# Kernel tuning notes

Measured on AMD Instinct MI355X. Metric: run time of the kernel, lower is better.

Reference implementation:

```python
import jax, jax.numpy as jnp
import numpy as np

B, S, E = 4, 2048, 512
H, D = 8, 64  # n_head, attn_dim


def setup_inputs() -> dict:
    key = jax.random.key(0)
    ks = jax.random.split(key, 12)
    scale = 0.02
    return {
        "input_q": jax.random.normal(ks[0], (B, S, E), dtype=jnp.float32),
        "input_k": jax.random.normal(ks[1], (B, S, E), dtype=jnp.float32),
        "input_v": jax.random.normal(ks[2], (B, S, E), dtype=jnp.float32),
        "mask": jax.random.randint(ks[3], (B, S, S), 0, 2, dtype=jnp.int32),
        "wq": jax.random.normal(ks[4], (E, H * D), dtype=jnp.float32) * scale,
        "bq": jnp.zeros((H * D,), dtype=jnp.float32),
        "wk": jax.random.normal(ks[5], (E, H * D), dtype=jnp.float32) * scale,
        "bk": jnp.zeros((H * D,), dtype=jnp.float32),
        "wv": jax.random.normal(ks[6], (E, H * D), dtype=jnp.float32) * scale,
        "bv": jnp.zeros((H * D,), dtype=jnp.float32),
        "wo": jax.random.normal(ks[7], (H * D, E), dtype=jnp.float32) * scale,
        "bo": jnp.zeros((E,), dtype=jnp.float32),
    }


def reference(input_q, input_k, input_v, mask, wq, bq, wk, bk, wv, bv, wo, bo):
    b, lq, _ = input_q.shape
    lk = input_k.shape[1]
    # projections -> [b, len, H, D] -> [b, H, len, D]
    q = (input_q @ wq + bq).reshape(b, lq, H, D).transpose(0, 2, 1, 3)
    k = (input_k @ wk + bk).reshape(b, lk, H, D).transpose(0, 2, 1, 3)
    v = (input_v @ wv + bv).reshape(b, lk, H, D).transpose(0, 2, 1, 3)
    # raw scores [b, H, lq, lk]
    score = jnp.einsum("bhqd,bhkd->bhqk", q, k)
    # NOTE: original masks with -1e9 BEFORE dividing by sqrt(attn_dim)
    score = jnp.where(mask[:, None, :, :] == 0, jnp.float32(-1e9), score)
    attn = jax.nn.softmax(score / jnp.sqrt(jnp.float32(D)), axis=-1)
    out = jnp.einsum("bhqk,bhkd->bqhd", attn, v).reshape(b, lq, H * D)
    return out @ wo + bo
```

## Files before the change

### kernel.cpp

```cpp
#include <hip/hip_runtime.h>
#include <hip/hip_bf16.h>
#include <hip/hip_fp16.h>
#include <stdint.h>

#define Bc 4
#define Sc 2048
#define Ec 512
#define Hc 8
#define Dc 64
#define HDc 512

typedef __attribute__((ext_vector_type(8))) short bf16x8;
typedef __attribute__((ext_vector_type(2))) _Float16 f16x2;
typedef __attribute__((ext_vector_type(4))) _Float16 f16x4;
typedef __attribute__((ext_vector_type(8))) _Float16 f16x8;
typedef __attribute__((ext_vector_type(4))) float f32x4;
typedef __attribute__((ext_vector_type(16))) float f32x16;
typedef unsigned int u32;

__device__ __forceinline__ unsigned short f2bf(float x) {
    union { float f; unsigned u; } v; v.f = x;
    unsigned r = v.u + 0x7FFFu + ((v.u >> 16) & 1u);
    return (unsigned short)(r >> 16);
}

__device__ __forceinline__ unsigned pkbf2(float a, float b) {
    float2 f; f.x = a; f.y = b;
    __hip_bfloat162 h = __float22bfloat162_rn(f);
    union { __hip_bfloat162 h2; unsigned u; } u; u.h2 = h;
    return u.u;
}

__device__ __forceinline__ unsigned short f2h(float x) {
    return __half_as_ushort(__float2half_rn(x));
}

__device__ __forceinline__ unsigned pkh2(float a, float b) {
    union { __half2 h2; unsigned u; } u;
    u.h2 = __floats2half2_rn(a, b);
    return u.u;
}

__device__ __forceinline__ uint4 pack8(float4 a, float4 b) {
    uint4 v;
    v.x = pkbf2(a.x, a.y); v.y = pkbf2(a.z, a.w);
    v.z = pkbf2(b.x, b.y); v.w = pkbf2(b.z, b.w);
    return v;
}

__device__ __forceinline__ void gload_lds(const void* g, void* l) {
    __builtin_amdgcn_global_load_lds(
        (const __attribute__((address_space(1))) u32*)g,
        (__attribute__((address_space(3))) u32*)l,
        16, 0, 0);
}

__global__ __launch_bounds__(256) void prep(
    const int* __restrict__ mask, unsigned long long* __restrict__ bits,
    const float* __restrict__ W0, const float* __restrict__ W1,
    const float* __restrict__ W2, const float* __restrict__ W3,
    unsigned short* __restrict__ Wt,
    const float* __restrict__ Xq, const float* __restrict__ Xk,
    const float* __restrict__ Xv, unsigned short* __restrict__ Xb)
{
    const int blk = blockIdx.x;
    __shared__ float t[64][65];
    if (blk < 256) {
        const int z = blk >> 6;
        const float* W = z == 0 ? W0 : (z == 1 ? W1 : (z == 2 ? W2 : W3));
        unsigned short* O = Wt + (size_t)z * Ec * HDc;
        const int k0 = ((blk >> 3) & 7) * 64, n0 = (blk & 7) * 64;
#pragma unroll
        for (int i = 0; i < 16; i++) {
            int idx = threadIdx.x + 256 * i;
            int kr = idx >> 6, nc = idx & 63;
            t[nc][kr] = W[(size_t)(k0 + kr) * HDc + n0 + nc];
        }
        __syncthreads();
#pragma unroll
        for (int i = 0; i < 16; i++) {
            int idx = threadIdx.x + 256 * i;
            int nr = idx >> 6, kc = idx & 63;
            O[(size_t)(n0 + nr) * Ec + k0 + kc] = f2bf(t[nr][kc]);
        }
    } else if (blk < 2304) {
        const int lane = threadIdx.x & 63;
        int wave = ((blk - 256) * 256 + (int)threadIdx.x) >> 6;
        const int nwaves = (2048 * 256) >> 6;
        const int nwords = (Bc * Sc * Sc) / 64;
        for (int w = wave; w < nwords; w += nwaves) {
            int m = mask[(size_t)w * 64 + lane];
            unsigned long long b = __ballot(m != 0);
            if (lane == 0) bits[w] = b;
        }
    } else {
        const int zi = blk - 2304;
        const int z = zi >> 11, wi = zi & 2047;
        const float* X = z == 0 ? Xq : (z == 1 ? Xk : Xv);
        const size_t off = ((size_t)wi * 256 + threadIdx.x) * 8;
        const float4* p = (const float4*)(X + off);
        float4 f0 = p[0], f1 = p[1];
        *(uint4*)(Xb + (size_t)z * 4194304 + off) = pack8(f0, f1);
    }
}

__global__ __launch_bounds__(256) void proj_gemm(
    const unsigned short* __restrict__ Xb, const unsigned short* __restrict__ Wt,
    const float* __restrict__ bq, const float* __restrict__ bk, const float* __restrict__ bv,
    unsigned short* __restrict__ Oq, unsigned short* __restrict__ Ok,
    unsigned short* __restrict__ Vt)
{
    const int z = blockIdx.z;
    const unsigned short* Xz = Xb + (size_t)z * 4194304;
    const unsigned short* Bt = Wt + (size_t)z * Ec * HDc;
    const float* bias = z == 0 ? bq : (z == 1 ? bk : bv);

    const int n0 = blockIdx.x * 128;
    const int m0 = blockIdx.y * 128;
    const int tid = threadIdx.x, lane = tid & 63, w = tid >> 6;
    const int c = lane & 15, quad = lane >> 4;
    const int wm = w & 1, wn = w >> 1;

    __shared__ unsigned short As[128 * 64];
    __shared__ unsigned short Bs[128 * 64];

    f32x4 acc[4][4];
#pragma unroll
    for (int i = 0; i < 4; i++)
#pragma unroll
        for (int j = 0; j < 4; j++) acc[i][j] = (f32x4){0.f, 0.f, 0.f, 0.f};

    for (int k0 = 0; k0 < Ec; k0 += 64) {
        __syncthreads();
#pragma unroll
        for (int jj = 0; jj < 4; jj++) {
            int rb = w * 32 + jj * 8;
            int row = rb + (lane >> 3);
            int dg = (lane & 7) ^ (row & 7);
            gload_lds(Bt + (size_t)(n0 + row) * Ec + k0 + dg * 8, &Bs[rb * 64]);
            gload_lds(Xz + (size_t)(m0 + row) * Ec + k0 + dg * 8, &As[rb * 64]);
        }
        __syncthreads();
#pragma unroll
        for (int ks = 0; ks < 2; ks++) {
            int kg = ks * 4 + quad;
            bf16x8 af[4], bfr[4];
#pragma unroll
            for (int mt = 0; mt < 4; mt++) {
                int row = wm * 64 + mt * 16 + c;
                af[mt] = *(const bf16x8*)&As[row * 64 + ((kg ^ (row & 7)) * 8)];
            }
#pragma unroll
            for (int nt = 0; nt < 4; nt++) {
                int row = wn * 64 + nt * 16 + c;
                bfr[nt] = *(const bf16x8*)&Bs[row * 64 + ((kg ^ (row & 7)) * 8)];
            }
            if (z < 2) {
#pragma unroll
                for (int mt = 0; mt < 4; mt++)
#pragma unroll
                    for (int nt = 0; nt < 4; nt++)
                        acc[mt][nt] = __builtin_amdgcn_mfma_f32_16x16x32_bf16(af[mt], bfr[nt], acc[mt][nt], 0, 0, 0);
            } else {
#pragma unroll
                for (int mt = 0; mt < 4; mt++)
#pragma unroll
                    for (int nt = 0; nt < 4; nt++)
                        acc[mt][nt] = __builtin_amdgcn_mfma_f32_16x16x32_bf16(bfr[nt], af[mt], acc[mt][nt], 0, 0, 0);
            }
        }
    }

    if (z < 2) {
        unsigned short* O = z == 0 ? Oq : Ok;
        const float qs = z == 0 ? 0.125f : 1.0f;
#pragma unroll
        for (int mt = 0; mt < 4; mt++)
#pragma unroll
            for (int r = 0; r < 4; r++) {
                int gm = m0 + wm * 64 + mt * 16 + quad * 4 + r;
#pragma unroll
                for (int nt = 0; nt < 4; nt++) {
                    int gn = n0 + wn * 64 + nt * 16 + c;
                    O[(size_t)gm * HDc + gn] = f2bf((acc[mt][nt][r] + bias[gn]) * qs);
                }
            }
    } else {
#pragma unroll
        for (int mt = 0; mt < 4; mt++) {
            int gm = m0 + wm * 64 + mt * 16 + c;
            int bb = gm >> 11, sPos = gm & (Sc - 1);
#pragma unroll
            for (int nt = 0; nt < 4; nt++)
#pragma unroll
                for (int r = 0; r < 4; r++) {
                    int ng = n0 + wn * 64 + nt * 16 + quad * 4 + r;
                    int hh = ng >> 6, d = ng & 63;
                    Vt[((size_t)(bb * Hc + hh) * Dc + d) * Sc + sPos] = f2h(acc[mt][nt][r] + bias[ng]);
                }
        }
    }
}

__global__ __launch_bounds__(256, 4) void attn_kernel(
    const unsigned short* __restrict__ Qb, const unsigned short* __restrict__ Kb,
    const unsigned short* __restrict__ Vt, const unsigned long long* __restrict__ Mb,
    unsigned short* __restrict__ Ob)
{
    const int flat = blockIdx.x + 32 * blockIdx.y + 256 * blockIdx.z;
    const int hb = flat & 7;
    const int qt = (flat >> 3) & 31;
    const int b  = flat >> 8;
    const int q0 = qt * 64;
    const int tid = threadIdx.x, lane = tid & 63, w = tid >> 6;
    const int l31 = lane & 31, hf = lane >> 5;
    const int half = w >> 1;
    const int qgrp = w & 1;

    __shared__ unsigned short SM[16384];
    unsigned short* KsH = SM + half * 4096;
    unsigned short* VsH = SM + 8192 + half * 4096;

    const int qg = q0 + qgrp * 32 + l31;
    const size_t qoff = ((size_t)b * Sc + qg) * HDc + hb * Dc;

    bf16x8 qf[4];
#pragma unroll
    for (int s4 = 0; s4 < 4; s4++)
        qf[s4] = *(const bf16x8*)(Qb + qoff + s4 * 16 + hf * 8);

    const unsigned long long* mr = Mb + ((size_t)b * Sc + qg) * (Sc / 64);
    const size_t kbase = ((size_t)b * Sc) * HDc + hb * Dc;
    const size_t vbase = ((size_t)(b * Hc + hb)) * Dc * Sc;

    f32x16 o[2];
#pragma unroll
    for (int i = 0; i < 16; i++) { o[0][i] = 0.f; o[1][i] = 0.f; }
    float os[4] = {0.f, 0.f, 0.f, 0.f};
    const f16x2 one2 = {(_Float16)1.0f, (_Float16)1.0f};

    auto stage = [&](int t) {
#pragma unroll
        for (int jj = 0; jj < 4; jj++) {
            int rb = qgrp * 32 + jj * 8;
            int row = rb + (lane >> 3);
            int dg = (lane & 7) ^ (row & 7);
            gload_lds(Kb + kbase + (size_t)(t * 64 + row) * HDc + dg * 8, &KsH[rb * 64]);
            gload_lds(Vt + vbase + (size_t)row * Sc + t * 64 + dg * 8, &VsH[rb * 64]);
        }
    };

    for (int i = 0; i < 16; i++) {
        const int t = half * 16 + i;
        unsigned long long mw = mr[t];
        stage(t);
        __syncthreads();

        u32 P16[2][8];
#pragma unroll
        for (int a = 0; a < 2; a++) {
            f32x16 s;
#pragma unroll
            for (int i2 = 0; i2 < 16; i2++) s[i2] = 0.f;
            const int tk = a * 32 + l31;
#pragma unroll
            for (int s4 = 0; s4 < 4; s4++) {
                bf16x8 kf = *(const bf16x8*)&KsH[tk * 64 + (((2 * s4 + hf) ^ (tk & 7)) * 8)];
                s = __builtin_amdgcn_mfma_f32_32x32x16_bf16(kf, qf[s4], s, 0, 0, 0);
            }
            u32 mwa = (a == 0) ? (u32)mw : (u32)(mw >> 32);
            int mq = (int)(mwa >> (4 * hf));
#pragma unroll
            for (int g = 0; g < 4; g++) {
                float p[4];
#pragma unroll
                for (int r = 0; r < 4; r++) {
                    const int pos = 8 * g + r;
                    int keep = __builtin_amdgcn_sbfe(mq, pos, 1);
                    float e = __expf(s[4 * g + r]);
                    p[r] = __int_as_float(__float_as_int(e) & keep);
                }
                u32 u0 = pkh2(p[0], p[1]);
                u32 u1 = pkh2(p[2], p[3]);
                P16[a][2 * g + 0] = u0;
                P16[a][2 * g + 1] = u1;
                union { u32 u; f16x2 h; } d0, d1;
                d0.u = u0; d1.u = u1;
                os[g] = __builtin_amdgcn_fdot2(d0.h, one2, os[g], false);
                os[g] = __builtin_amdgcn_fdot2(d1.h, one2, os[g], false);
            }
        }

        u32 pw[4][4];
#pragma unroll
        for (int s4 = 0; s4 < 4; s4++) {
            const int a = s4 >> 1, base = 4 * (s4 & 1);
#pragma unroll
            for (int pp = 0; pp < 2; pp++) {
                u32 A0 = P16[a][base + pp];
                u32 B1 = P16[a][base + 2 + pp];
                u32 sent = hf ? A0 : B1;
                u32 got = (u32)__shfl_xor((int)sent, 32, 64);
                pw[s4][pp]     = hf ? got : A0;
                pw[s4][2 + pp] = hf ? B1  : got;
            }
        }
#pragma unroll
        for (int s4 = 0; s4 < 4; s4++) {
            union { u32 u[4]; f16x8 v; } pf;
            pf.u[0] = pw[s4][0]; pf.u[1] = pw[s4][1];
            pf.u[2] = pw[s4][2]; pf.u[3] = pw[s4][3];
#pragma unroll
            for (int dt = 0; dt < 2; dt++) {
                const int d = dt * 32 + l31;
                f16x8 vf = *(const f16x8*)&VsH[d * 64 + (((2 * s4 + hf) ^ (d & 7)) * 8)];
                o[dt] = __builtin_amdgcn_mfma_f32_32x32x16_f16(vf, pf.v, o[dt], 0, 0, 0);
            }
        }
        __syncthreads();
    }

    float osum = os[0] + os[1] + os[2] + os[3];
    osum += __shfl_xor(osum, 32, 64);

    float* mbuf = (float*)SM;
    if (half == 1) {
        float* mp = mbuf + (qgrp * 64 + lane) * 34;
#pragma unroll
        for (int dt = 0; dt < 2; dt++)
#pragma unroll
            for (int i = 0; i < 16; i++) mp[dt * 16 + i] = o[dt][i];
        mp[32] = osum;
    }
    __syncthreads();
    if (half == 0) {
        const float* mp = mbuf + (qgrp * 64 + lane) * 34;
#pragma unroll
        for (int dt = 0; dt < 2; dt++)
#pragma unroll
            for (int i = 0; i < 16; i++) o[dt][i] += mp[dt * 16 + i];
        const float inv = 1.0f / (osum + mp[32]);
#pragma unroll
        for (int dt = 0; dt < 2; dt++)
#pragma unroll
            for (int g = 0; g < 4; g++) {
                const int d = dt * 32 + 8 * g + 4 * hf;
                uint2 pk;
                pk.x = pkbf2(o[dt][4 * g + 0] * inv, o[dt][4 * g + 1] * inv);
                pk.y = pkbf2(o[dt][4 * g + 2] * inv, o[dt][4 * g + 3] * inv);
                *(uint2*)(Ob + qoff + d) = pk;
            }
    }
}

__global__ __launch_bounds__(256) void out_gemm(
    const unsigned short* __restrict__ Ab, const unsigned short* __restrict__ Bt,
    const float* __restrict__ bias, float* __restrict__ Out)
{
    const int n0 = blockIdx.x * 128;
    const int m0 = blockIdx.y * 64;
    const int tid = threadIdx.x, lane = tid & 63, w = tid >> 6;
    const int c = lane & 15, quad = lane >> 4;
    const int wm = w & 1, wn = w >> 1;

    __shared__ unsigned short As[64 * 64];
    __shared__ unsigned short Bs[128 * 64];

    f32x4 acc[2][4];
#pragma unroll
    for (int i = 0; i < 2; i++)
#pragma unroll
        for (int j = 0; j < 4; j++) acc[i][j] = (f32x4){0.f, 0.f, 0.f, 0.f};

    for (int k0 = 0; k0 < HDc; k0 += 64) {
        __syncthreads();
#pragma unroll
        for (int jj = 0; jj < 4; jj++) {
            int rb = w * 32 + jj * 8;
            int row = rb + (lane >> 3);
            int dg = (lane & 7) ^ (row & 7);
            gload_lds(Bt + (size_t)(n0 + row) * Ec + k0 + dg * 8, &Bs[rb * 64]);
        }
#pragma unroll
        for (int jj = 0; jj < 2; jj++) {
            int rb = w * 16 + jj * 8;
            int row = rb + (lane >> 3);
            int dg = (lane & 7) ^ (row & 7);
            gload_lds(Ab + (size_t)(m0 + row) * HDc + k0 + dg * 8, &As[rb * 64]);
        }
        __syncthreads();
#pragma unroll
        for (int ks = 0; ks < 2; ks++) {
            int kg = ks * 4 + quad;
            bf16x8 af[2], bfr[4];
#pragma unroll
            for (int mt = 0; mt < 2; mt++) {
                int row = wm * 32 + mt * 16 + c;
                af[mt] = *(const bf16x8*)&As[row * 64 + ((kg ^ (row & 7)) * 8)];
            }
#pragma unroll
            for (int nt = 0; nt < 4; nt++) {
                int row = wn * 64 + nt * 16 + c;
                bfr[nt] = *(const bf16x8*)&Bs[row * 64 + ((kg ^ (row & 7)) * 8)];
            }
#pragma unroll
            for (int mt = 0; mt < 2; mt++)
#pragma unroll
                for (int nt = 0; nt < 4; nt++)
                    acc[mt][nt] = __builtin_amdgcn_mfma_f32_16x16x32_bf16(af[mt], bfr[nt], acc[mt][nt], 0, 0, 0);
        }
    }
#pragma unroll
    for (int mt = 0; mt < 2; mt++)
#pragma unroll
        for (int r = 0; r < 4; r++) {
            int gm = m0 + wm * 32 + mt * 16 + quad * 4 + r;
#pragma unroll
            for (int nt = 0; nt < 4; nt++) {
                int gn = n0 + wn * 64 + nt * 16 + c;
                Out[(size_t)gm * Ec + gn] = acc[mt][nt][r] + bias[gn];
            }
        }
}

extern "C" void kernel_launch(void* const* d_in, const int* in_sizes, int n_in,
                              void* d_out, int out_size, void* d_ws, size_t ws_size,
                              hipStream_t stream)
{
    const float* xq = (const float*)d_in[0];
    const float* xk = (const float*)d_in[1];
    const float* xv = (const float*)d_in[2];
    const int* mask = (const int*)d_in[3];
    const float* wq = (const float*)d_in[4];
    const float* bq = (const float*)d_in[5];
    const float* wk = (const float*)d_in[6];
    const float* bk = (const float*)d_in[7];
    const float* wv = (const float*)d_in[8];
    const float* bv = (const float*)d_in[9];
    const float* wo = (const float*)d_in[10];
    const float* bo = (const float*)d_in[11];
    float* out = (float*)d_out;

    char* ws = (char*)d_ws;
    const size_t MB = 1024 * 1024;
    unsigned short* qb = (unsigned short*)(ws + 0 * MB);
    unsigned short* kb = (unsigned short*)(ws + 8 * MB);
    unsigned short* vt = (unsigned short*)(ws + 16 * MB);
    unsigned short* xb = (unsigned short*)(ws + 24 * MB);
    unsigned short* ab = (unsigned short*)(ws + 24 * MB);
    unsigned long long* mb = (unsigned long long*)(ws + 48 * MB);
    unsigned short* wt = (unsigned short*)(ws + 50 * MB);

    hipLaunchKernelGGL(prep, dim3(8448), dim3(256), 0, stream,
                       mask, mb, wq, wk, wv, wo, wt, xq, xk, xv, xb);

    hipLaunchKernelGGL(proj_gemm, dim3(4, 64, 3), dim3(256), 0, stream,
                       xb, wt, bq, bk, bv, qb, kb, vt);

    hipLaunchKernelGGL(attn_kernel, dim3(32, 8, 4), dim3(256), 0, stream,
                       qb, kb, vt, mb, ab);

    hipLaunchKernelGGL(out_gemm, dim3(4, 128), dim3(256), 0, stream,
                       ab, wt + 3 * (size_t)Ec * HDc, bo, out);
}
```

Baseline: 269.2 us.

## Double-buffer K/V tiles in attention with smaller key tiles and exp2 softmax

```diff
diff --git a/kernel.cpp b/kernel.cpp
--- a/kernel.cpp
+++ b/kernel.cpp
@@ -173,7 +173,7 @@
 
     if (z < 2) {
         unsigned short* O = z == 0 ? Oq : Ok;
-        const float qs = z == 0 ? 0.125f : 1.0f;
+        const float qs = z == 0 ? 0.18033688011112043f : 1.0f;
 #pragma unroll
         for (int mt = 0; mt < 4; mt++)
 #pragma unroll
@@ -218,8 +218,8 @@
     const int qgrp = w & 1;
 
     __shared__ unsigned short SM[16384];
-    unsigned short* KsH = SM + half * 4096;
-    unsigned short* VsH = SM + 8192 + half * 4096;
+    unsigned short* Kb0 = SM + half * 4096;
+    unsigned short* Vb0 = SM + 8192 + half * 4096;
 
     const int qg = q0 + qgrp * 32 + l31;
     const size_t qoff = ((size_t)b * Sc + qg) * HDc + hb * Dc;
@@ -229,9 +229,10 @@
     for (int s4 = 0; s4 < 4; s4++)
         qf[s4] = *(const bf16x8*)(Qb + qoff + s4 * 16 + hf * 8);
 
-    const unsigned long long* mr = Mb + ((size_t)b * Sc + qg) * (Sc / 64);
+    const u32* mr32 = (const u32*)(Mb + ((size_t)b * Sc + qg) * (Sc / 64));
     const size_t kbase = ((size_t)b * Sc) * HDc + hb * Dc;
     const size_t vbase = ((size_t)(b * Hc + hb)) * Dc * Sc;
+    const int tok0 = half * 1024;
 
     f32x16 o[2];
 #pragma unroll
@@ -239,86 +240,102 @@
     float os[4] = {0.f, 0.f, 0.f, 0.f};
     const f16x2 one2 = {(_Float16)1.0f, (_Float16)1.0f};
 
-    auto stage = [&](int t) {
-#pragma unroll
-        for (int jj = 0; jj < 4; jj++) {
-            int rb = qgrp * 32 + jj * 8;
-            int row = rb + (lane >> 3);
-            int dg = (lane & 7) ^ (row & 7);
-            gload_lds(Kb + kbase + (size_t)(t * 64 + row) * HDc + dg * 8, &KsH[rb * 64]);
-            gload_lds(Vt + vbase + (size_t)row * Sc + t * 64 + dg * 8, &VsH[rb * 64]);
+    auto stage = [&](int t, int buf) {
+        unsigned short* Kd = Kb0 + buf * 2048;
+        unsigned short* Vd = Vb0 + buf * 2048;
+#pragma unroll
+        for (int jj = 0; jj < 2; jj++) {
+            int rbk = qgrp * 16 + jj * 8;
+            int rowk = rbk + (lane >> 3);
+            int dgk = (lane & 7) ^ (rowk & 7);
+            gload_lds(Kb + kbase + (size_t)(tok0 + t * 32 + rowk) * HDc + dgk * 8,
+                      &Kd[rbk * 64]);
+            int rbv = qgrp * 32 + jj * 16;
+            int rowd = rbv + (lane >> 2);
+            int dgv = (lane & 3) ^ ((rowd >> 1) & 3);
+            gload_lds(Vt + vbase + (size_t)rowd * Sc + tok0 + t * 32 + dgv * 8,
+                      &Vd[rbv * 32]);
         }
     };
 
-    for (int i = 0; i < 16; i++) {
-        const int t = half * 16 + i;
-        unsigned long long mw = mr[t];
-        stage(t);
-        __syncthreads();
-
-        u32 P16[2][8];
-#pragma unroll
-        for (int a = 0; a < 2; a++) {
-            f32x16 s;
-#pragma unroll
-            for (int i2 = 0; i2 < 16; i2++) s[i2] = 0.f;
-            const int tk = a * 32 + l31;
-#pragma unroll
-            for (int s4 = 0; s4 < 4; s4++) {
-                bf16x8 kf = *(const bf16x8*)&KsH[tk * 64 + (((2 * s4 + hf) ^ (tk & 7)) * 8)];
-                s = __builtin_amdgcn_mfma_f32_32x32x16_bf16(kf, qf[s4], s, 0, 0, 0);
-            }
-            u32 mwa = (a == 0) ? (u32)mw : (u32)(mw >> 32);
-            int mq = (int)(mwa >> (4 * hf));
-#pragma unroll
-            for (int g = 0; g < 4; g++) {
-                float p[4];
-#pragma unroll
-                for (int r = 0; r < 4; r++) {
-                    const int pos = 8 * g + r;
-                    int keep = __builtin_amdgcn_sbfe(mq, pos, 1);
-                    float e = __expf(s[4 * g + r]);
-                    p[r] = __int_as_float(__float_as_int(e) & keep);
-                }
-                u32 u0 = pkh2(p[0], p[1]);
-                u32 u1 = pkh2(p[2], p[3]);
-                P16[a][2 * g + 0] = u0;
-                P16[a][2 * g + 1] = u1;
-                union { u32 u; f16x2 h; } d0, d1;
-                d0.u = u0; d1.u = u1;
-                os[g] = __builtin_amdgcn_fdot2(d0.h, one2, os[g], false);
-                os[g] = __builtin_amdgcn_fdot2(d1.h, one2, os[g], false);
-            }
-        }
-
-        u32 pw[4][4];
+    stage(0, 0);
+    u32 mw_cur = mr32[half * 32];
+    u32 mw_nxt = 0;
+#pragma unroll 2
+    for (int i = 0; i < 32; i++) {
+        const int cur = i & 1;
+        __syncthreads();
+        if (i + 1 < 32) {
+            stage(i + 1, cur ^ 1);
+            mw_nxt = mr32[half * 32 + i + 1];
+        }
+        const unsigned short* Kt = Kb0 + cur * 2048;
+        const unsigned short* Vl = Vb0 + cur * 2048;
+
+        f32x16 s;
+#pragma unroll
+        for (int i2 = 0; i2 < 16; i2++) s[i2] = 0.f;
+        __builtin_amdgcn_s_setprio(1);
 #pragma unroll
         for (int s4 = 0; s4 < 4; s4++) {
-            const int a = s4 >> 1, base = 4 * (s4 & 1);
+            bf16x8 kf = *(const bf16x8*)&Kt[l31 * 64 + (((2 * s4 + hf) ^ (l31 & 7)) * 8)];
+            s = __builtin_amdgcn_mfma_f32_32x32x16_bf16(kf, qf[s4], s, 0, 0, 0);
+        }
+        __builtin_amdgcn_s_setprio(0);
+
+        int mq = (int)(mw_cur >> (4 * hf));
+        u32 P16[8];
+#pragma unroll
+        for (int g = 0; g < 4; g++) {
+            float p[4];
+#pragma unroll
+            for (int r = 0; r < 4; r++) {
+                const int pos = 8 * g + r;
+                int keep = __builtin_amdgcn_sbfe(mq, pos, 1);
+                float e = __builtin_exp2f(s[4 * g + r]);
+                p[r] = __int_as_float(__float_as_int(e) & keep);
+            }
+            u32 u0 = pkh2(p[0], p[1]);
+            u32 u1 = pkh2(p[2], p[3]);
+            P16[2 * g + 0] = u0;
+            P16[2 * g + 1] = u1;
+            union { u32 u; f16x2 h; } d0, d1;
+            d0.u = u0; d1.u = u1;
+            os[g] = __builtin_amdgcn_fdot2(d0.h, one2, os[g], false);
+            os[g] = __builtin_amdgcn_fdot2(d1.h, one2, os[g], false);
+        }
+
+        u32 pw[2][4];
+#pragma unroll
+        for (int s4 = 0; s4 < 2; s4++) {
+            const int base = 4 * s4;
 #pragma unroll
             for (int pp = 0; pp < 2; pp++) {
-                u32 A0 = P16[a][base + pp];
-                u32 B1 = P16[a][base + 2 + pp];
+                u32 A0 = P16[base + pp];
+                u32 B1 = P16[base + 2 + pp];
                 u32 sent = hf ? A0 : B1;
                 u32 got = (u32)__shfl_xor((int)sent, 32, 64);
                 pw[s4][pp]     = hf ? got : A0;
                 pw[s4][2 + pp] = hf ? B1  : got;
             }
         }
-#pragma unroll
-        for (int s4 = 0; s4 < 4; s4++) {
+        __builtin_amdgcn_s_setprio(1);
+#pragma unroll
+        for (int s4 = 0; s4 < 2; s4++) {
             union { u32 u[4]; f16x8 v; } pf;
             pf.u[0] = pw[s4][0]; pf.u[1] = pw[s4][1];
             pf.u[2] = pw[s4][2]; pf.u[3] = pw[s4][3];
 #pragma unroll
             for (int dt = 0; dt < 2; dt++) {
                 const int d = dt * 32 + l31;
-                f16x8 vf = *(const f16x8*)&VsH[d * 64 + (((2 * s4 + hf) ^ (d & 7)) * 8)];
+                f16x8 vf = *(const f16x8*)&Vl[d * 32 + (((2 * s4 + hf) ^ ((d >> 1) & 3)) * 8)];
                 o[dt] = __builtin_amdgcn_mfma_f32_32x32x16_f16(vf, pf.v, o[dt], 0, 0, 0);
             }
         }
-        __syncthreads();
-    }
+        __builtin_amdgcn_s_setprio(0);
+        mw_cur = mw_nxt;
+    }
+    __syncthreads();
 
     float osum = os[0] + os[1] + os[2] + os[3];
     osum += __shfl_xor(osum, 32, 64);
```

Result: slower. 275.9 us (+2.5%).
